# Performance work log

Hardware: AMD Instinct MI355X
Metric: run time of the kernel (lower is better)

## Reference

```python
import jax, jax.numpy as jnp
import numpy as np

B, C, F = 4, 3, 51
H_OUT, W_OUT = 384, 384
H_IN, W_IN = H_OUT + F - 1, W_OUT + F - 1


def setup_inputs() -> dict:
    key = jax.random.key(0)
    k1, k2, k3 = jax.random.split(key, 3)
    tenIn = jax.random.normal(k1, (B, C, H_IN, W_IN), dtype=jnp.float32)
    tenVer = jax.random.uniform(k2, (B, F, H_OUT, W_OUT), dtype=jnp.float32)
    tenHor = jax.random.uniform(k3, (B, F, H_OUT, W_OUT), dtype=jnp.float32)
    return {"tenIn": tenIn, "tenVer": tenVer, "tenHor": tenHor}


def reference(tenIn, tenVer, tenHor):
    # Out[n,c,y,x] = sum_{fy,fx} In[n,c,y+fy,x+fx] * Ver[n,fy,y,x] * Hor[n,fx,y,x]
    b, c, h_in, w_in = tenIn.shape
    f = tenVer.shape[1]
    h_out, w_out = tenVer.shape[2], tenVer.shape[3]

    # Horizontal sliding windows of the input, built once (static slices):
    # wx[b,c,fx,y_in,x] = In[b,c,y_in,x+fx]  -> [B,C,F,H_in,W_out]
    wx = jnp.stack([tenIn[:, :, :, fx:fx + w_out] for fx in range(f)], axis=2)

    def step(acc, fy):
        # rows[b,c,fx,y,x] = In[b,c,y+fy,x+fx]  -> [B,C,F,H_out,W_out]
        rows = jax.lax.dynamic_slice_in_dim(wx, fy, h_out, axis=3)
        # horizontal contraction with per-pixel horizontal kernel
        a = jnp.einsum('bcfyx,bfyx->bcyx', rows, tenHor)
        # weight by per-pixel vertical kernel tap fy
        ver_fy = jax.lax.dynamic_slice_in_dim(tenVer, fy, 1, axis=1)  # [B,1,H,W]
        return acc + a * ver_fy, None

    out0 = jnp.zeros((b, c, h_out, w_out), dtype=tenIn.dtype)
    out, _ = jax.lax.scan(step, out0, jnp.arange(f))
    return out
```

## Files before the change

### kernel.cpp

```cpp
#include <hip/hip_runtime.h>

namespace {
constexpr int CC = 3, FF = 51;
constexpr int BB = 4;
constexpr int HOUT = 384, WOUT = 384;
constexpr int HIN = 434, WIN = 434;
constexpr int KY = 4;
constexpr int LANES = 64;
constexpr int NW = 4;
constexpr int EXT = LANES + FF - 1;
constexpr int LPAD = 128;
constexpr int NSTEP = FF + KY - 1;
constexpr int NSG = CC * LPAD / LANES;
constexpr int NQW = 4;
constexpr int NPW = 8;
constexpr int SSTRIDE = NW * CC * LPAD;

using half2v = _Float16 __attribute__((ext_vector_type(2)));

__device__ __forceinline__ float fdot2f(half2v a, half2v b, float c) {
#if __has_builtin(__builtin_amdgcn_fdot2)
  return __builtin_amdgcn_fdot2(a, b, c, false);
#else
  return c + (float)a.x * (float)b.x + (float)a.y * (float)b.y;
#endif
}
}

__global__ __launch_bounds__(NW* LANES, 2) void sepconv_kernel(
    const float* __restrict__ In, const float* __restrict__ Ver,
    const float* __restrict__ Hor, float* __restrict__ Out) {
  const int lane = threadIdx.x;
  const int w = threadIdx.y;
  const int x0 = blockIdx.x * LANES;
  const int y0 = blockIdx.y * KY;
  const int b = blockIdx.z;
  const int x = x0 + lane;
  const int fxBase = 13 * w;
  const int ntaps = (w < 3) ? 13 : 12;
  const int aw = (lane + fxBase) & 3;
  const int bw = lane + fxBase - aw;

  __shared__ __align__(16) unsigned short sIn[2][NW][CC][LPAD];
  __shared__ float sRed[NW - 1][CC][KY][LANES];
  unsigned short* const sflat = &sIn[0][0][0][0];

  const size_t HW = (size_t)HOUT * WOUT;

  half2v hp[KY][NPW];
  {
    const float* horx = Hor + (size_t)b * FF * HW + x;
#pragma unroll
    for (int t = 0; t < KY; ++t) {
      const float* hb = horx + (size_t)(y0 + t) * WOUT;
#pragma unroll
      for (int j = 0; j < NPW; ++j) {
        const int u0 = 2 * j - aw;
        const int u1 = u0 + 1;
        float f0 = (u0 >= 0 && u0 < ntaps) ? hb[(size_t)(fxBase + u0) * HW] : 0.0f;
        float f1 = (u1 >= 0 && u1 < ntaps) ? hb[(size_t)(fxBase + u1) * HW] : 0.0f;
        half2v p;
        p.x = (_Float16)f0;
        p.y = (_Float16)f1;
        hp[t][j] = p;
      }
    }
  }

  const float* inb = In + ((size_t)b * CC * HIN + y0) * WIN + x0;
  const float* verb = Ver + (size_t)b * FF * HW + (size_t)y0 * WOUT + x;

  float acc[CC][KY] = {};
  float sv[NSG];
  float vvA[KY], vvB[KY];

#define STAGE_LOAD(R)                                                         \
  _Pragma("unroll") for (int k = 0; k < NSG; ++k) {                           \
    const int e = lane + (k & 1) * 64;                                        \
    const bool valid = ((k & 1) == 0) || (lane < EXT - LANES);                \
    sv[k] = valid ? inb[(size_t)((k >> 1) * HIN + (R)) * WIN + e] : 0.0f;     \
  }

#define STAGE_WRITE(BF)                                                       \
  _Pragma("unroll") for (int k = 0; k < NSG; ++k) {                           \
    const int e = lane + (k & 1) * 64;                                        \
    sflat[(BF)*SSTRIDE + (w * CC + (k >> 1)) * LPAD + e] =                    \
        __builtin_bit_cast(unsigned short, (_Float16)sv[k]);                  \
  }

#define VV_G(R, V)                                                            \
  _Pragma("unroll") for (int t = 0; t < KY; ++t) {                            \
    const int u = (R)-t;                                                      \
    V[t] = (u >= 0 && u < FF)                                                 \
               ? verb[(size_t)u * HW + (size_t)t * WOUT]                      \
               : 0.0f;                                                        \
  }

#define COMPUTE(BF, V)                                                        \
  {                                                                           \
    _Pragma("unroll") for (int c = 0; c < CC; ++c) {                          \
      const unsigned short* rp = sflat + (BF)*SSTRIDE + (w * CC + c) * LPAD + bw; \
      float d[KY];                                                            \
      {                                                                       \
        const uint2 u2 = *reinterpret_cast<const uint2*>(rp);                 \
        const half2v p0 = __builtin_bit_cast(half2v, u2.x);                   \
        const half2v p1 = __builtin_bit_cast(half2v, u2.y);                   \
        _Pragma("unroll") for (int t = 0; t < KY; ++t) {                      \
          d[t] = fdot2f(p0, hp[t][0], 0.0f);                                  \
          d[t] = fdot2f(p1, hp[t][1], d[t]);                                  \
        }                                                                     \
      }                                                                       \
      _Pragma("unroll") for (int q = 1; q < NQW; ++q) {                       \
        const uint2 u2 = *reinterpret_cast<const uint2*>(rp + 4 * q);         \
        const half2v p0 = __builtin_bit_cast(half2v, u2.x);                   \
        const half2v p1 = __builtin_bit_cast(half2v, u2.y);                   \
        _Pragma("unroll") for (int t = 0; t < KY; ++t) {                      \
          d[t] = fdot2f(p0, hp[t][2 * q], d[t]);                              \
          d[t] = fdot2f(p1, hp[t][2 * q + 1], d[t]);                          \
        }                                                                     \
      }                                                                       \
      _Pragma("unroll") for (int t = 0; t < KY; ++t)                          \
        acc[c][t] = __builtin_fmaf(d[t], V[t], acc[c][t]);                    \
    }                                                                         \
  }

  STAGE_LOAD(0);
  STAGE_WRITE(0);
  VV_G(0, vvA);

#pragma unroll 1
  for (int r = 0; r < NSTEP; r += 2) {
    const bool more = (r + 2 < NSTEP);
    STAGE_LOAD(r + 1);
    VV_G(r + 1, vvB);
    COMPUTE(0, vvA);
    STAGE_WRITE(1);
    if (more) {
      STAGE_LOAD(r + 2);
      VV_G(r + 2, vvA);
    }
    COMPUTE(1, vvB);
    if (more) { STAGE_WRITE(0); }
  }

  if (w > 0) {
#pragma unroll
    for (int c = 0; c < CC; ++c)
#pragma unroll
      for (int t = 0; t < KY; ++t) sRed[w - 1][c][t][lane] = acc[c][t];
  }
  __syncthreads();
  if (w == 0) {
    float* outb = Out + (size_t)b * CC * HW + (size_t)y0 * WOUT + x0 + lane;
#pragma unroll
    for (int c = 0; c < CC; ++c)
#pragma unroll
      for (int t = 0; t < KY; ++t)
        outb[(size_t)c * HW + (size_t)t * WOUT] =
            acc[c][t] + sRed[0][c][t][lane] + sRed[1][c][t][lane] +
            sRed[2][c][t][lane];
  }
#undef STAGE_LOAD
#undef STAGE_WRITE
#undef VV_G
#undef COMPUTE
}

extern "C" void kernel_launch(void* const* d_in, const int* in_sizes, int n_in,
                              void* d_out, int out_size, void* d_ws, size_t ws_size,
                              hipStream_t stream) {
  const float* In = (const float*)d_in[0];
  const float* Ver = (const float*)d_in[1];
  const float* Hor = (const float*)d_in[2];
  float* Out = (float*)d_out;

  dim3 grid(WOUT / LANES, HOUT / KY, BB);
  dim3 block(LANES, NW, 1);
  sepconv_kernel<<<grid, block, 0, stream>>>(In, Ver, Hor, Out);
}
```

Baseline: 167.0 us.

## Loop over multiple row tiles per block and deepen input prefetch pipeline

Result: slower. 188.6 us (+12.9%).

```diff
diff --git a/kernel.cpp b/kernel.cpp
--- a/kernel.cpp
+++ b/kernel.cpp
@@ -6,6 +6,7 @@
 constexpr int HOUT = 384, WOUT = 384;
 constexpr int HIN = 434, WIN = 434;
 constexpr int KY = 4;
+constexpr int TILES = 3;
 constexpr int LANES = 64;
 constexpr int NW = 4;
 constexpr int EXT = LANES + FF - 1;
@@ -33,7 +34,6 @@
   const int lane = threadIdx.x;
   const int w = threadIdx.y;
   const int x0 = blockIdx.x * LANES;
-  const int y0 = blockIdx.y * KY;
   const int b = blockIdx.z;
   const int x = x0 + lane;
   const int fxBase = 13 * w;
@@ -47,45 +47,21 @@
 
   const size_t HW = (size_t)HOUT * WOUT;
 
-  half2v hp[KY][NPW];
-  {
-    const float* horx = Hor + (size_t)b * FF * HW + x;
-#pragma unroll
-    for (int t = 0; t < KY; ++t) {
-      const float* hb = horx + (size_t)(y0 + t) * WOUT;
-#pragma unroll
-      for (int j = 0; j < NPW; ++j) {
-        const int u0 = 2 * j - aw;
-        const int u1 = u0 + 1;
-        float f0 = (u0 >= 0 && u0 < ntaps) ? hb[(size_t)(fxBase + u0) * HW] : 0.0f;
-        float f1 = (u1 >= 0 && u1 < ntaps) ? hb[(size_t)(fxBase + u1) * HW] : 0.0f;
-        half2v p;
-        p.x = (_Float16)f0;
-        p.y = (_Float16)f1;
-        hp[t][j] = p;
-      }
-    }
-  }
-
-  const float* inb = In + ((size_t)b * CC * HIN + y0) * WIN + x0;
-  const float* verb = Ver + (size_t)b * FF * HW + (size_t)y0 * WOUT + x;
-
-  float acc[CC][KY] = {};
-  float sv[NSG];
+  float sA[NSG], sB[NSG];
   float vvA[KY], vvB[KY];
 
-#define STAGE_LOAD(R)                                                         \
+#define STAGE_LOAD(R, SV)                                                     \
   _Pragma("unroll") for (int k = 0; k < NSG; ++k) {                           \
     const int e = lane + (k & 1) * 64;                                        \
     const bool valid = ((k & 1) == 0) || (lane < EXT - LANES);                \
-    sv[k] = valid ? inb[(size_t)((k >> 1) * HIN + (R)) * WIN + e] : 0.0f;     \
+    SV[k] = valid ? inb[(size_t)((k >> 1) * HIN + (R)) * WIN + e] : 0.0f;     \
   }
 
-#define STAGE_WRITE(BF)                                                       \
+#define STAGE_WRITE(BF, SV)                                                   \
   _Pragma("unroll") for (int k = 0; k < NSG; ++k) {                           \
     const int e = lane + (k & 1) * 64;                                        \
     sflat[(BF)*SSTRIDE + (w * CC + (k >> 1)) * LPAD + e] =                    \
-        __builtin_bit_cast(unsigned short, (_Float16)sv[k]);                  \
+        __builtin_bit_cast(unsigned short, (_Float16)SV[k]);                  \
   }
 
 #define VV_G(R, V)                                                            \
@@ -124,41 +100,75 @@
     }                                                                         \
   }
 
-  STAGE_LOAD(0);
-  STAGE_WRITE(0);
-  VV_G(0, vvA);
+#pragma unroll 1
+  for (int ty = 0; ty < TILES; ++ty) {
+    const int y0 = (blockIdx.y * TILES + ty) * KY;
+
+    const float* inb = In + ((size_t)b * CC * HIN + y0) * WIN + x0;
+    const float* verb = Ver + (size_t)b * FF * HW + (size_t)y0 * WOUT + x;
+
+    half2v hp[KY][NPW];
+    {
+      const float* horx = Hor + (size_t)b * FF * HW + x;
+#pragma unroll
+      for (int t = 0; t < KY; ++t) {
+        const float* hb = horx + (size_t)(y0 + t) * WOUT;
+#pragma unroll
+        for (int j = 0; j < NPW; ++j) {
+          const int u0 = 2 * j - aw;
+          const int u1 = u0 + 1;
+          float f0 =
+              (u0 >= 0 && u0 < ntaps) ? hb[(size_t)(fxBase + u0) * HW] : 0.0f;
+          float f1 =
+              (u1 >= 0 && u1 < ntaps) ? hb[(size_t)(fxBase + u1) * HW] : 0.0f;
+          half2v p;
+          p.x = (_Float16)f0;
+          p.y = (_Float16)f1;
+          hp[t][j] = p;
+        }
+      }
+    }
+
+    float acc[CC][KY] = {};
+
+    STAGE_LOAD(0, sA);
+    STAGE_WRITE(0, sA);
+    STAGE_LOAD(1, sB);
+    STAGE_LOAD(2, sA);
+    VV_G(0, vvA);
 
 #pragma unroll 1
-  for (int r = 0; r < NSTEP; r += 2) {
-    const bool more = (r + 2 < NSTEP);
-    STAGE_LOAD(r + 1);
-    VV_G(r + 1, vvB);
-    COMPUTE(0, vvA);
-    STAGE_WRITE(1);
-    if (more) {
-      STAGE_LOAD(r + 2);
+    for (int r = 0; r < NSTEP; r += 2) {
+      const int rB = (r + 3 < NSTEP) ? r + 3 : NSTEP - 1;
+      const int rA = (r + 4 < NSTEP) ? r + 4 : NSTEP - 1;
+      STAGE_WRITE(1, sB);
+      STAGE_LOAD(rB, sB);
+      VV_G(r + 1, vvB);
+      COMPUTE(0, vvA);
+      STAGE_WRITE(0, sA);
+      STAGE_LOAD(rA, sA);
       VV_G(r + 2, vvA);
+      COMPUTE(1, vvB);
     }
-    COMPUTE(1, vvB);
-    if (more) { STAGE_WRITE(0); }
-  }
 
-  if (w > 0) {
+    __syncthreads();
+    if (w > 0) {
 #pragma unroll
-    for (int c = 0; c < CC; ++c)
+      for (int c = 0; c < CC; ++c)
 #pragma unroll
-      for (int t = 0; t < KY; ++t) sRed[w - 1][c][t][lane] = acc[c][t];
-  }
-  __syncthreads();
-  if (w == 0) {
-    float* outb = Out + (size_t)b * CC * HW + (size_t)y0 * WOUT + x0 + lane;
+        for (int t = 0; t < KY; ++t) sRed[w - 1][c][t][lane] = acc[c][t];
+    }
+    __syncthreads();
+    if (w == 0) {
+      float* outb = Out + (size_t)b * CC * HW + (size_t)y0 * WOUT + x0 + lane;
 #pragma unroll
-    for (int c = 0; c < CC; ++c)
+      for (int c = 0; c < CC; ++c)
 #pragma unroll
-      for (int t = 0; t < KY; ++t)
-        outb[(size_t)c * HW + (size_t)t * WOUT] =
-            acc[c][t] + sRed[0][c][t][lane] + sRed[1][c][t][lane] +
-            sRed[2][c][t][lane];
+        for (int t = 0; t < KY; ++t)
+          outb[(size_t)c * HW + (size_t)t * WOUT] =
+              acc[c][t] + sRed[0][c][t][lane] + sRed[1][c][t][lane] +
+              sRed[2][c][t][lane];
+    }
   }
 #undef STAGE_LOAD
 #undef STAGE_WRITE
@@ -174,7 +184,7 @@
   const float* Hor = (const float*)d_in[2];
   float* Out = (float*)d_out;
 
-  dim3 grid(WOUT / LANES, HOUT / KY, BB);
+  dim3 grid(WOUT / LANES, HOUT / (KY * TILES), BB);
   dim3 block(LANES, NW, 1);
   sepconv_kernel<<<grid, block, 0, stream>>>(In, Ver, Hor, Out);
 }
```

## Pre-convert input to padded fp16 and load windows straight into registers

Applied to the files above, without the earlier changes.

Result: slower. 181.6 us (+8.7%).

```diff
diff --git a/kernel.cpp b/kernel.cpp
--- a/kernel.cpp
+++ b/kernel.cpp
@@ -5,6 +5,7 @@
 constexpr int BB = 4;
 constexpr int HOUT = 384, WOUT = 384;
 constexpr int HIN = 434, WIN = 434;
+constexpr int WP = 448;
 constexpr int KY = 4;
 constexpr int LANES = 64;
 constexpr int NW = 4;
@@ -15,6 +16,7 @@
 constexpr int NQW = 4;
 constexpr int NPW = 8;
 constexpr int SSTRIDE = NW * CC * LPAD;
+constexpr size_t IN16_BYTES = (size_t)BB * CC * HIN * WP * 2;
 
 using half2v = _Float16 __attribute__((ext_vector_type(2)));
 
@@ -27,7 +29,153 @@
 }
 }
 
-__global__ __launch_bounds__(NW* LANES, 2) void sepconv_kernel(
+__global__ void cvt16_kernel(const float* __restrict__ in,
+                             unsigned int* __restrict__ out, int n2) {
+  int i = blockIdx.x * blockDim.x + threadIdx.x;
+  const int stride = gridDim.x * blockDim.x;
+  for (; i < n2; i += stride) {
+    const int row = i / (WP / 2);
+    const int p = i - row * (WP / 2);
+    unsigned int v = 0;
+    if (2 * p + 1 < WIN) {
+      const float2 f = *reinterpret_cast<const float2*>(
+          in + (size_t)row * WIN + 2 * p);
+      const unsigned short lo = __builtin_bit_cast(unsigned short, (_Float16)f.x);
+      const unsigned short hi = __builtin_bit_cast(unsigned short, (_Float16)f.y);
+      v = ((unsigned int)hi << 16) | lo;
+    }
+    out[i] = v;
+  }
+}
+
+__global__ __launch_bounds__(NW* LANES, 2) void sepconv_reg(
+    const float* __restrict__ Ver, const float* __restrict__ Hor,
+    float* __restrict__ Out, const unsigned short* __restrict__ In16) {
+  const int lane = threadIdx.x;
+  const int w = threadIdx.y;
+  const int x0 = blockIdx.x * LANES;
+  const int y0 = blockIdx.y * KY;
+  const int b = blockIdx.z;
+  const int x = x0 + lane;
+  const int fxBase = 13 * w;
+  const int ntaps = (w < 3) ? 13 : 12;
+  const int aw = (lane + fxBase) & 3;
+  const int bw = lane + fxBase - aw;
+
+  __shared__ float sRed[NW - 1][CC][KY][LANES];
+
+  const size_t HW = (size_t)HOUT * WOUT;
+
+  half2v hp[KY][NPW];
+  {
+    const float* horx = Hor + (size_t)b * FF * HW + x;
+#pragma unroll
+    for (int t = 0; t < KY; ++t) {
+      const float* hb = horx + (size_t)(y0 + t) * WOUT;
+#pragma unroll
+      for (int j = 0; j < NPW; ++j) {
+        const int u0 = 2 * j - aw;
+        const int u1 = u0 + 1;
+        float f0 = (u0 >= 0 && u0 < ntaps) ? hb[(size_t)(fxBase + u0) * HW] : 0.0f;
+        float f1 = (u1 >= 0 && u1 < ntaps) ? hb[(size_t)(fxBase + u1) * HW] : 0.0f;
+        half2v p;
+        p.x = (_Float16)f0;
+        p.y = (_Float16)f1;
+        hp[t][j] = p;
+      }
+    }
+  }
+
+  const unsigned short* inw[CC];
+#pragma unroll
+  for (int c = 0; c < CC; ++c)
+    inw[c] = In16 + (((size_t)b * CC + c) * HIN + y0) * WP + x0 + bw;
+
+  const float* verb = Ver + (size_t)b * FF * HW + (size_t)y0 * WOUT + x;
+
+  float acc[CC][KY] = {};
+  uint2 wA[CC][NQW], wB[CC][NQW];
+  float vvA[KY], vvB[KY];
+
+#define WLOAD(R, W)                                                           \
+  _Pragma("unroll") for (int c = 0; c < CC; ++c) {                            \
+    const unsigned short* pc = inw[c] + (size_t)(R)*WP;                       \
+    _Pragma("unroll") for (int q = 0; q < NQW; ++q)                           \
+      W[c][q] = *reinterpret_cast<const uint2*>(pc + 4 * q);                  \
+  }
+
+#define VV_G(R, V)                                                            \
+  _Pragma("unroll") for (int t = 0; t < KY; ++t) {                            \
+    const int u = (R)-t;                                                      \
+    V[t] = (u >= 0 && u < FF)                                                 \
+               ? verb[(size_t)u * HW + (size_t)t * WOUT]                      \
+               : 0.0f;                                                        \
+  }
+
+#define COMPUTEW(W, V)                                                        \
+  {                                                                           \
+    _Pragma("unroll") for (int c = 0; c < CC; ++c) {                          \
+      float d[KY];                                                            \
+      {                                                                       \
+        const half2v p0 = __builtin_bit_cast(half2v, W[c][0].x);              \
+        const half2v p1 = __builtin_bit_cast(half2v, W[c][0].y);              \
+        _Pragma("unroll") for (int t = 0; t < KY; ++t) {                      \
+          d[t] = fdot2f(p0, hp[t][0], 0.0f);                                  \
+          d[t] = fdot2f(p1, hp[t][1], d[t]);                                  \
+        }                                                                     \
+      }                                                                       \
+      _Pragma("unroll") for (int q = 1; q < NQW; ++q) {                       \
+        const half2v p0 = __builtin_bit_cast(half2v, W[c][q].x);              \
+        const half2v p1 = __builtin_bit_cast(half2v, W[c][q].y);              \
+        _Pragma("unroll") for (int t = 0; t < KY; ++t) {                      \
+          d[t] = fdot2f(p0, hp[t][2 * q], d[t]);                              \
+          d[t] = fdot2f(p1, hp[t][2 * q + 1], d[t]);                          \
+        }                                                                     \
+      }                                                                       \
+      _Pragma("unroll") for (int t = 0; t < KY; ++t)                          \
+        acc[c][t] = __builtin_fmaf(d[t], V[t], acc[c][t]);                    \
+    }                                                                         \
+  }
+
+  WLOAD(0, wA);
+  VV_G(0, vvA);
+
+#pragma unroll 1
+  for (int r = 0; r < NSTEP; r += 2) {
+    const bool more = (r + 2 < NSTEP);
+    WLOAD(r + 1, wB);
+    VV_G(r + 1, vvB);
+    COMPUTEW(wA, vvA);
+    if (more) {
+      WLOAD(r + 2, wA);
+      VV_G(r + 2, vvA);
+    }
+    COMPUTEW(wB, vvB);
+  }
+
+  if (w > 0) {
+#pragma unroll
+    for (int c = 0; c < CC; ++c)
+#pragma unroll
+      for (int t = 0; t < KY; ++t) sRed[w - 1][c][t][lane] = acc[c][t];
+  }
+  __syncthreads();
+  if (w == 0) {
+    float* outb = Out + (size_t)b * CC * HW + (size_t)y0 * WOUT + x0 + lane;
+#pragma unroll
+    for (int c = 0; c < CC; ++c)
+#pragma unroll
+      for (int t = 0; t < KY; ++t)
+        outb[(size_t)c * HW + (size_t)t * WOUT] =
+            acc[c][t] + sRed[0][c][t][lane] + sRed[1][c][t][lane] +
+            sRed[2][c][t][lane];
+  }
+#undef WLOAD
+#undef VV_G
+#undef COMPUTEW
+}
+
+__global__ __launch_bounds__(NW* LANES, 2) void sepconv_fb(
     const float* __restrict__ In, const float* __restrict__ Ver,
     const float* __restrict__ Hor, float* __restrict__ Out) {
   const int lane = threadIdx.x;
@@ -127,7 +275,6 @@
   STAGE_LOAD(0);
   STAGE_WRITE(0);
   VV_G(0, vvA);
-
 #pragma unroll 1
   for (int r = 0; r < NSTEP; r += 2) {
     const bool more = (r + 2 < NSTEP);
@@ -176,5 +323,13 @@
 
   dim3 grid(WOUT / LANES, HOUT / KY, BB);
   dim3 block(LANES, NW, 1);
-  sepconv_kernel<<<grid, block, 0, stream>>>(In, Ver, Hor, Out);
-}
+
+  if (ws_size >= IN16_BYTES && d_ws != nullptr) {
+    const int n2 = (int)((size_t)BB * CC * HIN * (WP / 2));
+    cvt16_kernel<<<2048, 256, 0, stream>>>(In, (unsigned int*)d_ws, n2);
+    sepconv_reg<<<grid, block, 0, stream>>>(Ver, Hor, Out,
+                                            (const unsigned short*)d_ws);
+  } else {
+    sepconv_fb<<<grid, block, 0, stream>>>(In, Ver, Hor, Out);
+  }
+}
```
